# Optimization experiments

Hardware: AMD Instinct MI355X
Metric: run time of the kernel (lower is better)

Reference implementation:

```python
import jax, jax.numpy as jnp
import numpy as np

N = 8192
D_IN, D_GAT, D_GCN = 128, 64, 64


def setup_inputs() -> dict:
    key = jax.random.key(0)
    ks = jax.random.split(key, 7)
    feat = jax.random.normal(ks[0], (N, D_IN), dtype=jnp.float32)
    r = jax.random.uniform(ks[1], (N, N), dtype=jnp.float32)
    sup = jnp.where(r < 0.01, r * 100.0, 0.0)
    xav = lambda k, shape: jax.random.normal(k, shape, dtype=jnp.float32) * jnp.sqrt(2.0 / (shape[0] + shape[1]))
    W_map = xav(ks[2], (D_IN, D_GAT))
    b_map = jnp.zeros((1,), dtype=jnp.float32)
    U = xav(ks[3], (D_GAT, 1))
    V = xav(ks[4], (D_GAT, 1))
    W_gcn = xav(ks[5], (D_GAT, D_GCN))
    return {"feat": feat, "sup": sup, "W_map": W_map, "b_map": b_map, "U": U, "V": V, "W_gcn": W_gcn}


def reference(feat, sup, W_map, b_map, U, V, W_gcn):
    n = sup.shape[0]
    sup2 = sup + jnp.eye(n, dtype=sup.dtype)  # add self-loops
    # GAT layer
    h = feat @ W_map                            # [N, D_GAT]
    s = h @ U                                   # [N, 1] score from source node i
    t = h @ V                                   # [N, 1] score from target node j
    # torch loop builds att[j, i] = tanh(s_i + t_j + b)
    att = jnp.tanh(s.T + t + b_map)             # [N, N]
    att = jnp.where(sup2 > 0, att, jnp.float32(-100.0))
    att = jax.nn.softmax(att, axis=1)
    gat_feat = jnp.tanh(att @ h)                # [N, D_GAT]
    # GCN layer (dropout is identity at inference)
    agg = sup2 @ gat_feat                       # [N, D_GAT]
    out = jax.nn.relu(agg @ W_gcn)              # [N, D_GCN]
    norm = jnp.linalg.norm(out, axis=1, keepdims=True)
    out = out / jnp.maximum(norm, jnp.float32(1e-12))  # F.normalize(p=2, dim=1)
    return out
```

## Files before the change

### kernel.cpp

```cpp
#include <hip/hip_runtime.h>


#define N_NODES 8192
#define D_IN    128
#define D_GAT   64
#define SLOTS   256
#define K1_BLOCKS (N_NODES / 4)
#define K2_BLOCKS (N_NODES / 4)

#define COMPACT4(VX, QQ)                                                      \
    {                                                                         \
        float ee[4] = {VX.x, VX.y, VX.z, VX.w};                               \
        _Pragma("unroll")                                                     \
        for (int u = 0; u < 4; ++u) {                                         \
            const int i = (QQ) * 4 + u;                                       \
            const float vv = ee[u] + ((i == j) ? 1.0f : 0.0f);      \
            const bool keep = vv > 0.f;                                       \
            const unsigned long long mask = __ballot(keep);                   \
            if (keep) {                                                       \
                const int pos = base +                                        \
                    __popcll(mask & ((1ull << lane) - 1ull));                 \
                if (pos < SLOTS) { colj[pos] = i; valj[pos] = vv; }           \
            }                                                                 \
            base += __popcll(mask);                                           \
        }                                                                     \
    }

__global__ __launch_bounds__(256) void k12_map_compact(
    const float* __restrict__ feat, const float* __restrict__ W_map,
    const float* __restrict__ U, const float* __restrict__ V,
    const float* __restrict__ sup,
    float* __restrict__ h, float* __restrict__ s, float* __restrict__ t,
    int* __restrict__ cnt, int* __restrict__ col, float* __restrict__ val)
{
    const int wid  = threadIdx.x >> 6;
    const int lane = threadIdx.x & 63;
    if (blockIdx.x < K1_BLOCKS) {
        const int row = blockIdx.x * 4 + wid;
        __shared__ float f[4 * D_IN];
        if (threadIdx.x < 128)
            ((float4*)f)[threadIdx.x] =
                ((const float4*)(feat + (size_t)blockIdx.x * 4 * D_IN))[threadIdx.x];
        __syncthreads();
        const float* fr = f + wid * D_IN;
        float acc = 0.f;
#pragma unroll 8
        for (int k = 0; k < D_IN; ++k)
            acc += fr[k] * W_map[k * D_GAT + lane];
        h[row * D_GAT + lane] = acc;
        float sv = acc * U[lane];
        float tv = acc * V[lane];
#pragma unroll
        for (int off = 32; off > 0; off >>= 1) {
            sv += __shfl_xor(sv, off);
            tv += __shfl_xor(tv, off);
        }
        if (lane == 0) { s[row] = sv; t[row] = tv; }
    } else {
        const int j = (blockIdx.x - K1_BLOCKS) * 4 + wid;
        int*   colj = col + j * SLOTS;
        float* valj = val + j * SLOTS;
        const float4* row4 = (const float4*)(sup + (size_t)j * N_NODES);
        int base = 0;
        for (int q = lane; q < N_NODES / 4; q += 128) {
            float4 v0 = row4[q];
            float4 v1 = row4[q + 64];
            COMPACT4(v0, q);
            COMPACT4(v1, q + 64);
        }
        if (lane == 0) cnt[j] = (base < SLOTS) ? base : SLOTS;
    }
}

__global__ __launch_bounds__(256) void k3_gat(
    const float* __restrict__ h, const float* __restrict__ s,
    const float* __restrict__ t, const float* __restrict__ b,
    const int* __restrict__ cnt, const int* __restrict__ col,
    float* __restrict__ gat)
{
    const int wid  = threadIdx.x >> 6;
    const int lane = threadIdx.x & 63;
    const int j = blockIdx.x * 4 + wid;
    const int m = cnt[j];
    const int* colj = col + j * SLOTS;
    __shared__ int   cl_s[4][SLOTS];
    __shared__ float w_s[4][SLOTS];
    int*   cl = cl_s[wid];
    float* w  = w_s[wid];
    const float tj = t[j] + b[0];

    float lmax = -1e30f;
    for (int p = lane; p < m; p += 64) {
        const int ci = colj[p];
        cl[p] = ci;
        const float e = tanhf(s[ci] + tj);
        w[p] = e;
        lmax = fmaxf(lmax, e);
    }
#pragma unroll
    for (int off = 32; off > 0; off >>= 1)
        lmax = fmaxf(lmax, __shfl_xor(lmax, off));

    float lsum = 0.f;
    for (int p = lane; p < m; p += 64) {
        const float e = __expf(w[p] - lmax);
        w[p] = e;
        lsum += e;
    }
#pragma unroll
    for (int off = 32; off > 0; off >>= 1) lsum += __shfl_xor(lsum, off);
    __syncthreads();

    const int c16 = (lane & 15) * 4;
    const int pp  = lane >> 4;
    float4 a0 = make_float4(0,0,0,0), a1 = a0, a2 = a0, a3 = a0;
    for (int base = 0; base < m; base += 16) {
        const int p0 = base + pp, p1 = p0 + 4, p2 = p0 + 8, p3 = p0 + 12;
        if (p0 < m) { const float wp = w[p0];
            const float4 v = *(const float4*)(h + cl[p0] * D_GAT + c16);
            a0.x += wp*v.x; a0.y += wp*v.y; a0.z += wp*v.z; a0.w += wp*v.w; }
        if (p1 < m) { const float wp = w[p1];
            const float4 v = *(const float4*)(h + cl[p1] * D_GAT + c16);
            a1.x += wp*v.x; a1.y += wp*v.y; a1.z += wp*v.z; a1.w += wp*v.w; }
        if (p2 < m) { const float wp = w[p2];
            const float4 v = *(const float4*)(h + cl[p2] * D_GAT + c16);
            a2.x += wp*v.x; a2.y += wp*v.y; a2.z += wp*v.z; a2.w += wp*v.w; }
        if (p3 < m) { const float wp = w[p3];
            const float4 v = *(const float4*)(h + cl[p3] * D_GAT + c16);
            a3.x += wp*v.x; a3.y += wp*v.y; a3.z += wp*v.z; a3.w += wp*v.w; }
    }
    float4 acc;
    acc.x = (a0.x + a1.x) + (a2.x + a3.x);
    acc.y = (a0.y + a1.y) + (a2.y + a3.y);
    acc.z = (a0.z + a1.z) + (a2.z + a3.z);
    acc.w = (a0.w + a1.w) + (a2.w + a3.w);
#pragma unroll
    for (int off = 16; off <= 32; off <<= 1) {
        acc.x += __shfl_xor(acc.x, off); acc.y += __shfl_xor(acc.y, off);
        acc.z += __shfl_xor(acc.z, off); acc.w += __shfl_xor(acc.w, off);
    }
    if (pp == 0) {
        const float inv = 1.0f / lsum;
        float4 o;
        o.x = tanhf(acc.x * inv); o.y = tanhf(acc.y * inv);
        o.z = tanhf(acc.z * inv); o.w = tanhf(acc.w * inv);
        *(float4*)(gat + j * D_GAT + c16) = o;
    }
}

__global__ __launch_bounds__(256) void k4_gcn(
    const float* __restrict__ gat, const float* __restrict__ W_gcn,
    const int* __restrict__ cnt, const int* __restrict__ col,
    const float* __restrict__ val, float* __restrict__ out)
{
    const int wid  = threadIdx.x >> 6;
    const int lane = threadIdx.x & 63;
    const int j = blockIdx.x * 4 + wid;
    const int m = cnt[j];
    const int*   colj = col + j * SLOTS;
    const float* valj = val + j * SLOTS;
    __shared__ int   cl_s[4][SLOTS];
    __shared__ float wv_s[4][SLOTS];
    __shared__ float a_s[4][D_GAT];
    int*   cl = cl_s[wid];
    float* wv = wv_s[wid];
    float* a  = a_s[wid];
    for (int p = lane; p < m; p += 64) { cl[p] = colj[p]; wv[p] = valj[p]; }
    __syncthreads();

    const int c16 = (lane & 15) * 4;
    const int pp  = lane >> 4;
    float4 a0 = make_float4(0,0,0,0), a1 = a0, a2 = a0, a3 = a0;
    for (int base = 0; base < m; base += 16) {
        const int p0 = base + pp, p1 = p0 + 4, p2 = p0 + 8, p3 = p0 + 12;
        if (p0 < m) { const float wp = wv[p0];
            const float4 v = *(const float4*)(gat + cl[p0] * D_GAT + c16);
            a0.x += wp*v.x; a0.y += wp*v.y; a0.z += wp*v.z; a0.w += wp*v.w; }
        if (p1 < m) { const float wp = wv[p1];
            const float4 v = *(const float4*)(gat + cl[p1] * D_GAT + c16);
            a1.x += wp*v.x; a1.y += wp*v.y; a1.z += wp*v.z; a1.w += wp*v.w; }
        if (p2 < m) { const float wp = wv[p2];
            const float4 v = *(const float4*)(gat + cl[p2] * D_GAT + c16);
            a2.x += wp*v.x; a2.y += wp*v.y; a2.z += wp*v.z; a2.w += wp*v.w; }
        if (p3 < m) { const float wp = wv[p3];
            const float4 v = *(const float4*)(gat + cl[p3] * D_GAT + c16);
            a3.x += wp*v.x; a3.y += wp*v.y; a3.z += wp*v.z; a3.w += wp*v.w; }
    }
    float4 acc;
    acc.x = (a0.x + a1.x) + (a2.x + a3.x);
    acc.y = (a0.y + a1.y) + (a2.y + a3.y);
    acc.z = (a0.z + a1.z) + (a2.z + a3.z);
    acc.w = (a0.w + a1.w) + (a2.w + a3.w);
#pragma unroll
    for (int off = 16; off <= 32; off <<= 1) {
        acc.x += __shfl_xor(acc.x, off); acc.y += __shfl_xor(acc.y, off);
        acc.z += __shfl_xor(acc.z, off); acc.w += __shfl_xor(acc.w, off);
    }
    if (pp == 0) *(float4*)(a + c16) = acc;
    __syncthreads();

    float o = 0.f;
#pragma unroll 8
    for (int d = 0; d < D_GAT; ++d)
        o += a[d] * W_gcn[d * D_GAT + lane];
    o = fmaxf(o, 0.f);

    float ss = o * o;
#pragma unroll
    for (int off = 32; off > 0; off >>= 1) ss += __shfl_xor(ss, off);
    const float nrm = sqrtf(ss);
    out[j * D_GAT + lane] = o / fmaxf(nrm, 1e-12f);
}

extern "C" void kernel_launch(void* const* d_in, const int* in_sizes, int n_in,
                              void* d_out, int out_size, void* d_ws, size_t ws_size,
                              hipStream_t stream) {
    const float* feat  = (const float*)d_in[0];
    const float* sup   = (const float*)d_in[1];
    const float* W_map = (const float*)d_in[2];
    const float* b_map = (const float*)d_in[3];
    const float* U     = (const float*)d_in[4];
    const float* V     = (const float*)d_in[5];
    const float* W_gcn = (const float*)d_in[6];
    float* out = (float*)d_out;

    char* ws = (char*)d_ws;
    float* h   = (float*)(ws);
    float* gat = (float*)(ws + (2u << 20));
    float* s   = (float*)(ws + (4u << 20));
    float* t   = (float*)(ws + (4u << 20) + 32768);
    int*   cnt = (int*)  (ws + (4u << 20) + 65536);
    int*   col = (int*)  (ws + (4u << 20) + 98304);
    float* val = (float*)(ws + (12u << 20) + 98304);

    k12_map_compact<<<K1_BLOCKS + K2_BLOCKS, 256, 0, stream>>>(
        feat, W_map, U, V, sup, h, s, t, cnt, col, val);
    k3_gat<<<N_NODES / 4, 256, 0, stream>>>(h, s, t, b_map, cnt, col, gat);
    k4_gcn<<<N_NODES / 4, 256, 0, stream>>>(gat, W_gcn, cnt, col, val, out);
}
```

Baseline: 413.0 us.

## Fuse adjacency compaction into GAT kernel, keep compacted row in LDS

The sparse-row compaction of the adjacency moves out of the combined map/compact kernel and into the GAT attention kernel. Each wave compacts its row into LDS and uses it directly for the softmax and aggregation, still writing col/val/cnt for the GCN kernel. This avoids the GAT kernel re-reading col indices from global memory. The cost is that the 256MB adjacency scan no longer overlaps with the small feature-mapping work. LDS per block also grows by one more 4x256 array.

```diff
diff --git a/kernel.cpp b/kernel.cpp
--- a/kernel.cpp
+++ b/kernel.cpp
@@ -5,8 +5,6 @@
 #define D_IN    128
 #define D_GAT   64
 #define SLOTS   256
-#define K1_BLOCKS (N_NODES / 4)
-#define K2_BLOCKS (N_NODES / 4)
 
 #define COMPACT4(VX, QQ)                                                      \
     {                                                                         \
@@ -20,83 +18,83 @@
             if (keep) {                                                       \
                 const int pos = base +                                        \
                     __popcll(mask & ((1ull << lane) - 1ull));                 \
-                if (pos < SLOTS) { colj[pos] = i; valj[pos] = vv; }           \
+                if (pos < SLOTS) { clr[pos] = i; vvr[pos] = vv; }             \
             }                                                                 \
             base += __popcll(mask);                                           \
         }                                                                     \
     }
 
-__global__ __launch_bounds__(256) void k12_map_compact(
+__global__ __launch_bounds__(256) void k1_map(
     const float* __restrict__ feat, const float* __restrict__ W_map,
     const float* __restrict__ U, const float* __restrict__ V,
-    const float* __restrict__ sup,
-    float* __restrict__ h, float* __restrict__ s, float* __restrict__ t,
-    int* __restrict__ cnt, int* __restrict__ col, float* __restrict__ val)
+    float* __restrict__ h, float* __restrict__ s, float* __restrict__ t)
 {
     const int wid  = threadIdx.x >> 6;
     const int lane = threadIdx.x & 63;
-    if (blockIdx.x < K1_BLOCKS) {
-        const int row = blockIdx.x * 4 + wid;
-        __shared__ float f[4 * D_IN];
-        if (threadIdx.x < 128)
-            ((float4*)f)[threadIdx.x] =
-                ((const float4*)(feat + (size_t)blockIdx.x * 4 * D_IN))[threadIdx.x];
-        __syncthreads();
-        const float* fr = f + wid * D_IN;
-        float acc = 0.f;
+    const int row = blockIdx.x * 4 + wid;
+    __shared__ float f[4 * D_IN];
+    if (threadIdx.x < 128)
+        ((float4*)f)[threadIdx.x] =
+            ((const float4*)(feat + (size_t)blockIdx.x * 4 * D_IN))[threadIdx.x];
+    __syncthreads();
+    const float* fr = f + wid * D_IN;
+    float acc = 0.f;
 #pragma unroll 8
-        for (int k = 0; k < D_IN; ++k)
-            acc += fr[k] * W_map[k * D_GAT + lane];
-        h[row * D_GAT + lane] = acc;
-        float sv = acc * U[lane];
-        float tv = acc * V[lane];
-#pragma unroll
-        for (int off = 32; off > 0; off >>= 1) {
-            sv += __shfl_xor(sv, off);
-            tv += __shfl_xor(tv, off);
-        }
-        if (lane == 0) { s[row] = sv; t[row] = tv; }
-    } else {
-        const int j = (blockIdx.x - K1_BLOCKS) * 4 + wid;
-        int*   colj = col + j * SLOTS;
-        float* valj = val + j * SLOTS;
-        const float4* row4 = (const float4*)(sup + (size_t)j * N_NODES);
-        int base = 0;
-        for (int q = lane; q < N_NODES / 4; q += 128) {
-            float4 v0 = row4[q];
-            float4 v1 = row4[q + 64];
-            COMPACT4(v0, q);
-            COMPACT4(v1, q + 64);
-        }
-        if (lane == 0) cnt[j] = (base < SLOTS) ? base : SLOTS;
-    }
-}
-
-__global__ __launch_bounds__(256) void k3_gat(
-    const float* __restrict__ h, const float* __restrict__ s,
-    const float* __restrict__ t, const float* __restrict__ b,
-    const int* __restrict__ cnt, const int* __restrict__ col,
+    for (int k = 0; k < D_IN; ++k)
+        acc += fr[k] * W_map[k * D_GAT + lane];
+    h[row * D_GAT + lane] = acc;
+    float sv = acc * U[lane];
+    float tv = acc * V[lane];
+#pragma unroll
+    for (int off = 32; off > 0; off >>= 1) {
+        sv += __shfl_xor(sv, off);
+        tv += __shfl_xor(tv, off);
+    }
+    if (lane == 0) { s[row] = sv; t[row] = tv; }
+}
+
+__global__ __launch_bounds__(256) void k23_compact_gat(
+    const float* __restrict__ sup, const float* __restrict__ h,
+    const float* __restrict__ s, const float* __restrict__ t,
+    const float* __restrict__ b,
+    int* __restrict__ cnt, int* __restrict__ col, float* __restrict__ val,
     float* __restrict__ gat)
 {
     const int wid  = threadIdx.x >> 6;
     const int lane = threadIdx.x & 63;
     const int j = blockIdx.x * 4 + wid;
-    const int m = cnt[j];
-    const int* colj = col + j * SLOTS;
+
     __shared__ int   cl_s[4][SLOTS];
+    __shared__ float vv_s[4][SLOTS];
     __shared__ float w_s[4][SLOTS];
-    int*   cl = cl_s[wid];
-    float* w  = w_s[wid];
+    int*   clr = cl_s[wid];
+    float* vvr = vv_s[wid];
+    float* w   = w_s[wid];
+
+    const float4* row4 = (const float4*)(sup + (size_t)j * N_NODES);
+    int base = 0;
+    for (int q = lane; q < N_NODES / 4; q += 128) {
+        float4 v0 = row4[q];
+        float4 v1 = row4[q + 64];
+        COMPACT4(v0, q);
+        COMPACT4(v1, q + 64);
+    }
+    const int m = (base < SLOTS) ? base : SLOTS;
+    __syncthreads();
+
+    int*   colj = col + j * SLOTS;
+    float* valj = val + j * SLOTS;
     const float tj = t[j] + b[0];
-
     float lmax = -1e30f;
     for (int p = lane; p < m; p += 64) {
-        const int ci = colj[p];
-        cl[p] = ci;
+        const int ci = clr[p];
+        colj[p] = ci;
+        valj[p] = vvr[p];
         const float e = tanhf(s[ci] + tj);
         w[p] = e;
         lmax = fmaxf(lmax, e);
     }
+    if (lane == 0) cnt[j] = m;
 #pragma unroll
     for (int off = 32; off > 0; off >>= 1)
         lmax = fmaxf(lmax, __shfl_xor(lmax, off));
@@ -114,19 +112,19 @@
     const int c16 = (lane & 15) * 4;
     const int pp  = lane >> 4;
     float4 a0 = make_float4(0,0,0,0), a1 = a0, a2 = a0, a3 = a0;
-    for (int base = 0; base < m; base += 16) {
-        const int p0 = base + pp, p1 = p0 + 4, p2 = p0 + 8, p3 = p0 + 12;
+    for (int bse = 0; bse < m; bse += 16) {
+        const int p0 = bse + pp, p1 = p0 + 4, p2 = p0 + 8, p3 = p0 + 12;
         if (p0 < m) { const float wp = w[p0];
-            const float4 v = *(const float4*)(h + cl[p0] * D_GAT + c16);
+            const float4 v = *(const float4*)(h + clr[p0] * D_GAT + c16);
             a0.x += wp*v.x; a0.y += wp*v.y; a0.z += wp*v.z; a0.w += wp*v.w; }
         if (p1 < m) { const float wp = w[p1];
-            const float4 v = *(const float4*)(h + cl[p1] * D_GAT + c16);
+            const float4 v = *(const float4*)(h + clr[p1] * D_GAT + c16);
             a1.x += wp*v.x; a1.y += wp*v.y; a1.z += wp*v.z; a1.w += wp*v.w; }
         if (p2 < m) { const float wp = w[p2];
-            const float4 v = *(const float4*)(h + cl[p2] * D_GAT + c16);
+            const float4 v = *(const float4*)(h + clr[p2] * D_GAT + c16);
             a2.x += wp*v.x; a2.y += wp*v.y; a2.z += wp*v.z; a2.w += wp*v.w; }
         if (p3 < m) { const float wp = w[p3];
-            const float4 v = *(const float4*)(h + cl[p3] * D_GAT + c16);
+            const float4 v = *(const float4*)(h + clr[p3] * D_GAT + c16);
             a3.x += wp*v.x; a3.y += wp*v.y; a3.z += wp*v.z; a3.w += wp*v.w; }
     }
     float4 acc;
@@ -233,8 +231,8 @@
     int*   col = (int*)  (ws + (4u << 20) + 98304);
     float* val = (float*)(ws + (12u << 20) + 98304);
 
-    k12_map_compact<<<K1_BLOCKS + K2_BLOCKS, 256, 0, stream>>>(
-        feat, W_map, U, V, sup, h, s, t, cnt, col, val);
-    k3_gat<<<N_NODES / 4, 256, 0, stream>>>(h, s, t, b_map, cnt, col, gat);
+    k1_map<<<N_NODES / 4, 256, 0, stream>>>(feat, W_map, U, V, h, s, t);
+    k23_compact_gat<<<N_NODES / 4, 256, 0, stream>>>(
+        sup, h, s, t, b_map, cnt, col, val, gat);
     k4_gcn<<<N_NODES / 4, 256, 0, stream>>>(gat, W_gcn, cnt, col, val, out);
 }
```

Result: no change. 406.2 us (-1.6%).
